# Kernel optimization log

Measured on AMD Instinct MI355X. Metric: run time of the kernel, lower is better.

Reference implementation:

```python
import jax, jax.numpy as jnp
import numpy as np

TOKENS, D_MODEL, N_EXPERTS, K = 16384, 4096, 64, 2


def setup_inputs() -> dict:
    key = jax.random.key(0)
    kx, kw, kb = jax.random.split(key, 3)
    x = jax.random.normal(kx, (TOKENS, D_MODEL), dtype=jnp.float32)
    # nn.Linear(input_dim, num_experts): weight [num_experts, input_dim], bias [num_experts]
    bound = 1.0 / np.sqrt(D_MODEL)
    W = jax.random.uniform(kw, (N_EXPERTS, D_MODEL), minval=-bound, maxval=bound, dtype=jnp.float32)
    b = jax.random.uniform(kb, (N_EXPERTS,), minval=-bound, maxval=bound, dtype=jnp.float32)
    return {"x": x, "W": W, "b": b}


def reference(x, W, b):
    # logits = x @ W.T + b ; softmax over experts ; top-k
    logits = jnp.einsum('td,ed->te', x, W) + b  # [tokens, experts]
    scores = jax.nn.softmax(logits, axis=-1)
    topk_scores, topk_indices = jax.lax.top_k(scores, K)
    return (topk_indices, topk_scores)
```

## Files before the change

kernel.cpp:

```cpp
#include <hip/hip_runtime.h>
#include <hip/hip_bf16.h>
#include <cstdint>
#include <cstddef>

#define TOKENS 16384
#define DMODEL 4096
#define NEXP   64
#define NWAVE  4
#define KSPAN  (DMODEL / NWAVE)
#define NKC    (KSPAN / 16)
#define NMAC   (NKC / 4)

typedef __attribute__((ext_vector_type(8)))  short bf16x8;
typedef __attribute__((ext_vector_type(16))) float f32x16;

__device__ __forceinline__ void cvt_hilo8(const float f[8], bf16x8* hi, bf16x8* lo) {
  union { __hip_bfloat16 b; unsigned short u; } cv;
  bf16x8 hv, lv;
#pragma unroll
  for (int j = 0; j < 8; ++j) {
    __hip_bfloat16 hb = __float2bfloat16(f[j]);
    cv.b = hb; hv[j] = (short)cv.u;
    float r = f[j] - __bfloat162float(hb);
    cv.b = __float2bfloat16(r); lv[j] = (short)cv.u;
  }
  *hi = hv; *lo = lv;
}

__global__ __launch_bounds__(256)
void prep_W(const float* __restrict__ W, uint4* __restrict__ wh, uint4* __restrict__ wl) {
  const int tid = blockIdx.x * 256 + threadIdx.x;
  const int l  = tid & 63;
  const int et = (tid >> 6) & 1;
  const int kc = tid >> 7;
  const int e  = et * 32 + (l & 31);
  const int k  = kc * 16 + (l >> 5) * 8;
  const float* src = W + (size_t)e * DMODEL + k;
  float f[8];
#pragma unroll
  for (int j = 0; j < 8; ++j) f[j] = src[j];
  bf16x8 hi, lo;
  cvt_hilo8(f, &hi, &lo);
  const int slot = (kc * 2 + et) * 64 + l;
  wh[slot] = __builtin_bit_cast(uint4, hi);
  wl[slot] = __builtin_bit_cast(uint4, lo);
}

__global__ __launch_bounds__(256, 2)
void gemm_topk(const float* __restrict__ x, const uint4* __restrict__ wh,
               const uint4* __restrict__ wl, const float* __restrict__ b,
               float* __restrict__ out) {
  __shared__ float red[NWAVE][32 * NEXP];

  const int tid = threadIdx.x;
  const int l   = tid & 63;
  const int w   = tid >> 6;
  const int t0  = blockIdx.x * 32;
  const int row = l & 31, g = l >> 5;

  const float* xp  = x  + (size_t)(t0 + row) * DMODEL + w * KSPAN + g * 8;
  const uint4* whp = wh + (size_t)w * (NKC * 128) + l;
  const uint4* wlp = wl + (size_t)w * (NKC * 128) + l;

  f32x16 acc0, acc1;
#pragma unroll
  for (int i = 0; i < 16; ++i) { acc0[i] = 0.f; acc1[i] = 0.f; }

  float4 xa[2][8];
  uint4  ph0[2], ph1[2], pl0[2], pl1[2];

  auto ldxm = [&](int kc0, int s) {
#pragma unroll
    for (int c = 0; c < 4; ++c) {
      const float* xn = xp + (size_t)(kc0 + c) * 16;
      xa[s][c * 2]     = *(const float4*)(xn);
      xa[s][c * 2 + 1] = *(const float4*)(xn + 4);
    }
  };
  auto ldw = [&](int kc, int s) {
    ph0[s] = whp[kc * 128];  ph1[s] = whp[kc * 128 + 64];
    pl0[s] = wlp[kc * 128];  pl1[s] = wlp[kc * 128 + 64];
  };

  auto chunk = [&](int kc, int xs, int c) {
    const int ws = kc & 1;
    float4 a0 = xa[xs][c * 2], a1 = xa[xs][c * 2 + 1];
    uint4 bh0 = ph0[ws], bh1 = ph1[ws], bl0 = pl0[ws], bl1 = pl1[ws];
    if (kc + 2 < NKC) ldw(kc + 2, ws);
    float f[8] = {a0.x, a0.y, a0.z, a0.w, a1.x, a1.y, a1.z, a1.w};
    bf16x8 ah, al;
    cvt_hilo8(f, &ah, &al);
    bf16x8 vh0 = __builtin_bit_cast(bf16x8, bh0);
    bf16x8 vh1 = __builtin_bit_cast(bf16x8, bh1);
    bf16x8 vl0 = __builtin_bit_cast(bf16x8, bl0);
    bf16x8 vl1 = __builtin_bit_cast(bf16x8, bl1);
    acc0 = __builtin_amdgcn_mfma_f32_32x32x16_bf16(ah, vh0, acc0, 0, 0, 0);
    acc1 = __builtin_amdgcn_mfma_f32_32x32x16_bf16(ah, vh1, acc1, 0, 0, 0);
    acc0 = __builtin_amdgcn_mfma_f32_32x32x16_bf16(ah, vl0, acc0, 0, 0, 0);
    acc1 = __builtin_amdgcn_mfma_f32_32x32x16_bf16(ah, vl1, acc1, 0, 0, 0);
    acc0 = __builtin_amdgcn_mfma_f32_32x32x16_bf16(al, vh0, acc0, 0, 0, 0);
    acc1 = __builtin_amdgcn_mfma_f32_32x32x16_bf16(al, vh1, acc1, 0, 0, 0);
  };

  ldxm(0, 0);
  ldw(0, 0); ldw(1, 1);

  for (int m = 0; m < NMAC; m += 2) {
    if (m + 1 < NMAC) ldxm((m + 1) * 4, 1);
#pragma unroll
    for (int c = 0; c < 4; ++c) chunk(m * 4 + c, 0, c);
    if (m + 2 < NMAC) ldxm((m + 2) * 4, 0);
#pragma unroll
    for (int c = 0; c < 4; ++c) chunk((m + 1) * 4 + c, 1, c);
  }

  {
    float* rp = &red[w][0];
#pragma unroll
    for (int r = 0; r < 16; ++r) {
      const int rr = (r & 3) + 8 * (r >> 2) + 4 * g;
      rp[rr * NEXP + row]      = acc0[r];
      rp[rr * NEXP + 32 + row] = acc1[r];
    }
  }
  __syncthreads();

  const float bias = b[tid & 63];
#pragma unroll
  for (int j = 0; j < 8; ++j) {
    const int f = tid + 256 * j;
    float s = red[0][f] + red[1][f] + red[2][f] + red[3][f] + bias;
    red[0][f] = s;
  }
  __syncthreads();

#pragma unroll
  for (int i = 0; i < 8; ++i) {
    const int tl = w * 8 + i;
    const float v = red[0][tl * NEXP + l];

    float m1 = v; int i1 = l;
#pragma unroll
    for (int off = 32; off > 0; off >>= 1) {
      float ov = __shfl_xor(m1, off, 64);
      int   oi = __shfl_xor(i1, off, 64);
      if (ov > m1 || (ov == m1 && oi < i1)) { m1 = ov; i1 = oi; }
    }
    float v2 = (l == i1) ? -__builtin_inff() : v;
    float m2 = v2; int i2 = l;
#pragma unroll
    for (int off = 32; off > 0; off >>= 1) {
      float ov = __shfl_xor(m2, off, 64);
      int   oi = __shfl_xor(i2, off, 64);
      if (ov > m2 || (ov == m2 && oi < i2)) { m2 = ov; i2 = oi; }
    }
    float e = __expf(v - m1);
#pragma unroll
    for (int off = 32; off > 0; off >>= 1) e += __shfl_xor(e, off, 64);

    if (l == 0) {
      const int t = t0 + tl;
      out[(size_t)t * 2 + 0] = (float)i1;
      out[(size_t)t * 2 + 1] = (float)i2;
      float inv = 1.0f / e;
      out[(size_t)TOKENS * 2 + (size_t)t * 2 + 0] = inv;
      out[(size_t)TOKENS * 2 + (size_t)t * 2 + 1] = __expf(m2 - m1) * inv;
    }
  }
}

extern "C" void kernel_launch(void* const* d_in, const int* in_sizes, int n_in,
                              void* d_out, int out_size, void* d_ws, size_t ws_size,
                              hipStream_t stream) {
  const float* x = (const float*)d_in[0];
  const float* W = (const float*)d_in[1];
  const float* b = (const float*)d_in[2];
  float* out = (float*)d_out;

  uint4* wh = (uint4*)d_ws;
  uint4* wl = wh + 32768;

  hipLaunchKernelGGL(prep_W,    dim3(128),         dim3(256), 0, stream, W, wh, wl);
  hipLaunchKernelGGL(gemm_topk, dim3(TOKENS / 32), dim3(256), 0, stream, x, wh, wl, b, out);
}
```

Measured before the change: 77.65 us.

## Stage x through swizzled double-buffered LDS with direct global-to-LDS loads

The kernel now copies x into LDS in 256-column windows using direct global-to-LDS 16-byte loads, double-buffered with barriers. Before, each wave streamed its own K-quarter from global memory into registers. Each wave now reads full contiguous 1 KB rows, and an XOR swizzle on the LDS layout avoids bank conflicts. The K split across waves becomes per-window instead of per-quarter. In exchange the kernel uses 64 KB of LDS per block and adds a barrier per window. The W fragments are now loaded at the start of each window with no cross-window prefetch, so their latency may be exposed.

```diff
diff --git a/kernel.cpp b/kernel.cpp
--- a/kernel.cpp
+++ b/kernel.cpp
@@ -7,12 +7,19 @@
 #define DMODEL 4096
 #define NEXP   64
 #define NWAVE  4
-#define KSPAN  (DMODEL / NWAVE)
-#define NKC    (KSPAN / 16)
-#define NMAC   (NKC / 4)
+#define WINK   256
+#define NWIN   (DMODEL / WINK)
+#define WCH    (WINK / 16)
+#define CPW    (WCH / NWAVE)
 
 typedef __attribute__((ext_vector_type(8)))  short bf16x8;
 typedef __attribute__((ext_vector_type(16))) float f32x16;
+
+__device__ __forceinline__ void gld_lds16(const float* g, void* l) {
+  __builtin_amdgcn_global_load_lds(
+      (__attribute__((address_space(1))) const void*)g,
+      (__attribute__((address_space(3))) void*)l, 16, 0, 0);
+}
 
 __device__ __forceinline__ void cvt_hilo8(const float f[8], bf16x8* hi, bf16x8* lo) {
   union { __hip_bfloat16 b; unsigned short u; } cv;
@@ -47,75 +54,81 @@
 }
 
 __global__ __launch_bounds__(256, 2)
-void gemm_topk(const float* __restrict__ x, const uint4* __restrict__ wh,
-               const uint4* __restrict__ wl, const float* __restrict__ b,
+void gemm_topk(const float* __restrict__ x, const uint4* __restrict__ whB,
+               const uint4* __restrict__ wlB, const float* __restrict__ b,
                float* __restrict__ out) {
-  __shared__ float red[NWAVE][32 * NEXP];
-
+  __shared__ __align__(16) char lds[65536];
   const int tid = threadIdx.x;
   const int l   = tid & 63;
   const int w   = tid >> 6;
   const int t0  = blockIdx.x * 32;
   const int row = l & 31, g = l >> 5;
 
-  const float* xp  = x  + (size_t)(t0 + row) * DMODEL + w * KSPAN + g * 8;
-  const uint4* whp = wh + (size_t)w * (NKC * 128) + l;
-  const uint4* wlp = wl + (size_t)w * (NKC * 128) + l;
+  char* xb0 = lds;
+  char* xb1 = lds + 32768;
+  const uint4* whp = whB + l;
+  const uint4* wlp = wlB + l;
+
+  auto stage = [&](int win, char* buf) {
+#pragma unroll
+    for (int p = 0; p < 8; ++p) {
+      const int r  = p * 4 + w;
+      const int sb = (l * 16) ^ ((r & 7) << 4);
+      const float* src = x + (size_t)(t0 + r) * DMODEL + win * WINK + (sb >> 2);
+      gld_lds16(src, buf + p * 4096 + tid * 16);
+    }
+  };
 
   f32x16 acc0, acc1;
 #pragma unroll
   for (int i = 0; i < 16; ++i) { acc0[i] = 0.f; acc1[i] = 0.f; }
 
-  float4 xa[2][8];
-  uint4  ph0[2], ph1[2], pl0[2], pl1[2];
-
-  auto ldxm = [&](int kc0, int s) {
+  auto compute = [&](const char* buf, int win) {
+    uint4 bh0[4], bh1[4], bl0[4], bl1[4];
 #pragma unroll
     for (int c = 0; c < 4; ++c) {
-      const float* xn = xp + (size_t)(kc0 + c) * 16;
-      xa[s][c * 2]     = *(const float4*)(xn);
-      xa[s][c * 2 + 1] = *(const float4*)(xn + 4);
+      const size_t base = (size_t)(win * WCH + w * CPW + c) * 128;
+      bh0[c] = whp[base];      bh1[c] = whp[base + 64];
+      bl0[c] = wlp[base];      bl1[c] = wlp[base + 64];
+    }
+#pragma unroll
+    for (int c = 0; c < 4; ++c) {
+      const int u = (w * CPW + c) * 4 + g * 2;
+      const int sw = (row & 7);
+      float4 a0 = *(const float4*)(buf + row * 1024 + ((u ^ sw) << 4));
+      float4 a1 = *(const float4*)(buf + row * 1024 + (((u + 1) ^ sw) << 4));
+      float f[8] = {a0.x, a0.y, a0.z, a0.w, a1.x, a1.y, a1.z, a1.w};
+      bf16x8 ah, al;
+      cvt_hilo8(f, &ah, &al);
+      bf16x8 vh0 = __builtin_bit_cast(bf16x8, bh0[c]);
+      bf16x8 vh1 = __builtin_bit_cast(bf16x8, bh1[c]);
+      bf16x8 vl0 = __builtin_bit_cast(bf16x8, bl0[c]);
+      bf16x8 vl1 = __builtin_bit_cast(bf16x8, bl1[c]);
+      acc0 = __builtin_amdgcn_mfma_f32_32x32x16_bf16(ah, vh0, acc0, 0, 0, 0);
+      acc1 = __builtin_amdgcn_mfma_f32_32x32x16_bf16(ah, vh1, acc1, 0, 0, 0);
+      acc0 = __builtin_amdgcn_mfma_f32_32x32x16_bf16(ah, vl0, acc0, 0, 0, 0);
+      acc1 = __builtin_amdgcn_mfma_f32_32x32x16_bf16(ah, vl1, acc1, 0, 0, 0);
+      acc0 = __builtin_amdgcn_mfma_f32_32x32x16_bf16(al, vh0, acc0, 0, 0, 0);
+      acc1 = __builtin_amdgcn_mfma_f32_32x32x16_bf16(al, vh1, acc1, 0, 0, 0);
     }
   };
-  auto ldw = [&](int kc, int s) {
-    ph0[s] = whp[kc * 128];  ph1[s] = whp[kc * 128 + 64];
-    pl0[s] = wlp[kc * 128];  pl1[s] = wlp[kc * 128 + 64];
-  };
 
-  auto chunk = [&](int kc, int xs, int c) {
-    const int ws = kc & 1;
-    float4 a0 = xa[xs][c * 2], a1 = xa[xs][c * 2 + 1];
-    uint4 bh0 = ph0[ws], bh1 = ph1[ws], bl0 = pl0[ws], bl1 = pl1[ws];
-    if (kc + 2 < NKC) ldw(kc + 2, ws);
-    float f[8] = {a0.x, a0.y, a0.z, a0.w, a1.x, a1.y, a1.z, a1.w};
-    bf16x8 ah, al;
-    cvt_hilo8(f, &ah, &al);
-    bf16x8 vh0 = __builtin_bit_cast(bf16x8, bh0);
-    bf16x8 vh1 = __builtin_bit_cast(bf16x8, bh1);
-    bf16x8 vl0 = __builtin_bit_cast(bf16x8, bl0);
-    bf16x8 vl1 = __builtin_bit_cast(bf16x8, bl1);
-    acc0 = __builtin_amdgcn_mfma_f32_32x32x16_bf16(ah, vh0, acc0, 0, 0, 0);
-    acc1 = __builtin_amdgcn_mfma_f32_32x32x16_bf16(ah, vh1, acc1, 0, 0, 0);
-    acc0 = __builtin_amdgcn_mfma_f32_32x32x16_bf16(ah, vl0, acc0, 0, 0, 0);
-    acc1 = __builtin_amdgcn_mfma_f32_32x32x16_bf16(ah, vl1, acc1, 0, 0, 0);
-    acc0 = __builtin_amdgcn_mfma_f32_32x32x16_bf16(al, vh0, acc0, 0, 0, 0);
-    acc1 = __builtin_amdgcn_mfma_f32_32x32x16_bf16(al, vh1, acc1, 0, 0, 0);
-  };
+  stage(0, xb0);
+  stage(1, xb1);
+  __syncthreads();
 
-  ldxm(0, 0);
-  ldw(0, 0); ldw(1, 1);
-
-  for (int m = 0; m < NMAC; m += 2) {
-    if (m + 1 < NMAC) ldxm((m + 1) * 4, 1);
-#pragma unroll
-    for (int c = 0; c < 4; ++c) chunk(m * 4 + c, 0, c);
-    if (m + 2 < NMAC) ldxm((m + 2) * 4, 0);
-#pragma unroll
-    for (int c = 0; c < 4; ++c) chunk((m + 1) * 4 + c, 1, c);
+  for (int wi = 0; wi < NWIN; wi += 2) {
+    compute(xb0, wi);
+    __syncthreads();
+    if (wi + 2 < NWIN) stage(wi + 2, xb0);
+    compute(xb1, wi + 1);
+    __syncthreads();
+    if (wi + 3 < NWIN) stage(wi + 3, xb1);
   }
 
+  float* red = (float*)lds;
   {
-    float* rp = &red[w][0];
+    float* rp = red + w * (32 * NEXP);
 #pragma unroll
     for (int r = 0; r < 16; ++r) {
       const int rr = (r & 3) + 8 * (r >> 2) + 4 * g;
@@ -129,15 +142,15 @@
 #pragma unroll
   for (int j = 0; j < 8; ++j) {
     const int f = tid + 256 * j;
-    float s = red[0][f] + red[1][f] + red[2][f] + red[3][f] + bias;
-    red[0][f] = s;
+    float s = red[f] + red[2048 + f] + red[4096 + f] + red[6144 + f] + bias;
+    red[f] = s;
   }
   __syncthreads();
 
 #pragma unroll
   for (int i = 0; i < 8; ++i) {
     const int tl = w * 8 + i;
-    const float v = red[0][tl * NEXP + l];
+    const float v = red[tl * NEXP + l];
 
     float m1 = v; int i1 = l;
 #pragma unroll
```

Result: slower. 85.10 us (+9.6%).
